# Kernel tuning notes

Measured on AMD Instinct MI355X. Metric: run time of the kernel, lower is better.

## Reference

```python
import jax, jax.numpy as jnp
import numpy as np

N_USERS = 100000
N_ITEMS = 50000
N_NODES = N_USERS + N_ITEMS
EMBED = 64
NNZ = 4000000
BATCH = 4096
N_LAYERS = 3


def setup_inputs() -> dict:
    key = jax.random.key(0)
    k = jax.random.split(key, 8)
    return {
        "batch_user": jax.random.randint(k[0], (BATCH,), 0, N_USERS),
        "batch_pos_item": jax.random.randint(k[1], (BATCH,), 0, N_ITEMS),
        "batch_neg_item": jax.random.randint(k[2], (BATCH,), 0, N_ITEMS),
        "embed_user": jax.random.normal(k[3], (N_USERS, EMBED), dtype=jnp.float32) * 0.1,
        "embed_item": jax.random.normal(k[4], (N_ITEMS, EMBED), dtype=jnp.float32) * 0.1,
        "row_idx": jax.random.randint(k[5], (NNZ,), 0, N_NODES),
        "col_idx": jax.random.randint(k[6], (NNZ,), 0, N_NODES),
        "a_vals": jax.random.uniform(k[7], (NNZ,), dtype=jnp.float32),
    }


def reference(batch_user, batch_pos_item, batch_neg_item,
              embed_user, embed_item, row_idx, col_idx, a_vals):
    # E: [N_NODES, D] stacked user+item embeddings
    E = jnp.concatenate([embed_user, embed_item], axis=0)
    acc = E
    for _ in range(N_LAYERS):
        # SpMM in COO form: out[r] += a[e] * E[c[e]]
        msgs = a_vals[:, None] * E[col_idx]            # [NNZ, D]
        E = jax.ops.segment_sum(msgs, row_idx, num_segments=N_NODES)
        acc = acc + E
    out = acc / (N_LAYERS + 1)
    user_g = out[:N_USERS]
    item_g = out[N_USERS:]
    return (user_g[batch_user], item_g[batch_pos_item], item_g[batch_neg_item])
```

## Files before the change

### kernel.cpp

```cpp
#include <hip/hip_runtime.h>

#define N_USERS 100000
#define N_ITEMS 50000
#define N_NODES 150000
#define EMBED   64
#define NNZV    4000000
#define BATCH   4096
#define BKW     586
#define NBKT    256
#define CAP     18304

__global__ __launch_bounds__(512) void k_parta(
        const int* __restrict__ row, const int* __restrict__ col,
        const float* __restrict__ vals, int* __restrict__ bcnt,
        unsigned long long* __restrict__ staging, int nnz) {
    __shared__ int cnt[NBKT];
    __shared__ int base_s[NBKT];
    int tid = threadIdx.x;
    if (tid < NBKT) cnt[tid] = 0;
    __syncthreads();
    int tile0 = blockIdx.x * 16384;
    for (int k = 0; k < 32; k++) {
        int e = tile0 + k * 512 + tid;
        if (e < nnz) atomicAdd(&cnt[row[e] / BKW], 1);
    }
    __syncthreads();
    if (tid < NBKT) {
        int c_ = cnt[tid];
        base_s[tid] = c_ ? (tid * CAP + atomicAdd(&bcnt[tid], c_)) : 0;
        cnt[tid] = 0;
    }
    __syncthreads();
    for (int k = 0; k < 32; k++) {
        int e = tile0 + k * 512 + tid;
        if (e < nnz) {
            int r = row[e];
            int b = r / BKW;
            int rank = atomicAdd(&cnt[b], 1);
            unsigned int key = ((unsigned int)(r - b * BKW) << 18) | (unsigned int)col[e];
            unsigned long long rec = (unsigned long long)key
                                   | ((unsigned long long)__float_as_uint(vals[e]) << 32);
            staging[base_s[b] + rank] = rec;
        }
    }
}

__global__ __launch_bounds__(512) void k_partb(
        const int* __restrict__ bcnt,
        const unsigned long long* __restrict__ staging,
        int* __restrict__ row_ptr,
        unsigned long long* __restrict__ edges) {
    __shared__ int s[512];
    __shared__ int cnt[BKW];
    __shared__ int cur[BKW];
    __shared__ int base_sh;
    int b = blockIdx.x;
    int t = threadIdx.x;

    int v = (t < NBKT) ? bcnt[t] : 0;
    s[t] = v;
    __syncthreads();
    for (int off = 1; off < 512; off <<= 1) {
        int u = (t >= off) ? s[t - off] : 0;
        __syncthreads();
        s[t] += u;
        __syncthreads();
    }
    if (t == b) base_sh = s[t] - v;
    if (b == 0 && t == 0) row_ptr[N_NODES] = NNZV;
    __syncthreads();
    int base = base_sh;
    int n    = bcnt[b];
    const unsigned long long* sb = staging + (size_t)b * CAP;

    int j0 = 2 * t, j1 = 2 * t + 1;
    if (j0 < BKW) cnt[j0] = 0;
    if (j1 < BKW) cnt[j1] = 0;
    __syncthreads();
    for (int i = t; i < n; i += 512)
        atomicAdd(&cnt[(unsigned int)sb[i] >> 18], 1);
    __syncthreads();
    int c0 = (j0 < BKW) ? cnt[j0] : 0;
    int c1 = (j1 < BKW) ? cnt[j1] : 0;
    int pair = c0 + c1;
    s[t] = pair;
    __syncthreads();
    for (int off = 1; off < 512; off <<= 1) {
        int u = (t >= off) ? s[t - off] : 0;
        __syncthreads();
        s[t] += u;
        __syncthreads();
    }
    int excl = s[t] - pair;
    if (j0 < BKW) cur[j0] = excl;
    if (j1 < BKW) cur[j1] = excl + c0;
    int r0 = b * BKW + j0;
    int r1 = b * BKW + j1;
    if (j0 < BKW && r0 < N_NODES) row_ptr[r0] = base + excl;
    if (j1 < BKW && r1 < N_NODES) row_ptr[r1] = base + excl + c0;
    __syncthreads();
    for (int i = t; i < n; i += 512) {
        unsigned long long rec = sb[i];
        unsigned int key = (unsigned int)rec;
        int rank = atomicAdd(&cur[key >> 18], 1);
        edges[base + rank] = (rec & 0xFFFFFFFF00000000ull) | (key & 0x3FFFFu);
    }
}

__device__ __forceinline__ float4 spmm_row(const int* row_ptr,
                                           const unsigned long long* edges,
                                           const float4* __restrict__ eu4,
                                           const float4* __restrict__ ei4s,
                                           int r, int lane) {
    int g = lane >> 4;
    int d = lane & 15;
    int start = row_ptr[r];
    int end   = row_ptr[r + 1];
    float4 acc = make_float4(0.f, 0.f, 0.f, 0.f);
    for (int e0 = start; e0 < end; e0 += 64) {
        int ei = e0 + lane;
        unsigned long long rec = 0ull;
        if (ei < end) rec = __builtin_nontemporal_load(edges + ei);
        int clo = (int)(rec & 0xffffffffull);
        int vhi = (int)(rec >> 32);
        int nleft = end - e0;
        int kmax = (nleft + 3) >> 2;
        #pragma unroll 4
        for (int k = 0; k < kmax; k++) {
            int src = 4 * k + g;
            int cc = __shfl(clo, src);
            float vv = __int_as_float(__shfl(vhi, src));
            const float4* basep = (cc < N_USERS) ? eu4 : ei4s;
            float4 e = basep[cc * 16 + d];
            acc.x += vv * e.x;
            acc.y += vv * e.y;
            acc.z += vv * e.z;
            acc.w += vv * e.w;
        }
    }
    acc.x += __shfl_xor(acc.x, 16);
    acc.y += __shfl_xor(acc.y, 16);
    acc.z += __shfl_xor(acc.z, 16);
    acc.w += __shfl_xor(acc.w, 16);
    acc.x += __shfl_xor(acc.x, 32);
    acc.y += __shfl_xor(acc.y, 32);
    acc.z += __shfl_xor(acc.z, 32);
    acc.w += __shfl_xor(acc.w, 32);
    return acc;
}

__global__ void k_spmm4(const int* __restrict__ row_ptr,
                        const unsigned long long* __restrict__ edges,
                        const float4* __restrict__ eu4,
                        const float4* __restrict__ ei4s,
                        float4* __restrict__ Eout) {
    int lane = threadIdx.x & 63;
    int wv   = threadIdx.x >> 6;
    int rbase = (blockIdx.x * 4 + wv) * 4;
    if (rbase >= N_NODES) return;
    int g = lane >> 4;
    int d = lane & 15;
    int st[4], en[4], len[4];
    #pragma unroll
    for (int i = 0; i < 4; i++) {
        int r = rbase + i;
        if (r < N_NODES) { st[i] = row_ptr[r]; en[i] = row_ptr[r + 1]; }
        else             { st[i] = 0;          en[i] = 0; }
        len[i] = en[i] - st[i];
    }
    int maxlen = len[0];
    #pragma unroll
    for (int i = 1; i < 4; i++) maxlen = (len[i] > maxlen) ? len[i] : maxlen;

    float4 acc[4];
    #pragma unroll
    for (int i = 0; i < 4; i++) acc[i] = make_float4(0.f, 0.f, 0.f, 0.f);

    for (int off = 0; off < maxlen; off += 64) {
        int clo[4], vhi[4], kmax[4];
        #pragma unroll
        for (int i = 0; i < 4; i++) {
            int ei = st[i] + off + lane;
            unsigned long long rec = 0ull;
            if (ei < en[i]) rec = __builtin_nontemporal_load(edges + ei);
            clo[i] = (int)(rec & 0xffffffffull);
            vhi[i] = (int)(rec >> 32);
            int nleft = len[i] - off;
            if (nleft < 0) nleft = 0; else if (nleft > 64) nleft = 64;
            kmax[i] = (nleft + 3) >> 2;
        }
        int kmx = (maxlen - off + 3) >> 2; if (kmx > 16) kmx = 16;
        #pragma unroll 4
        for (int k = 0; k < kmx; k++) {
            int src = 4 * k + g;
            #pragma unroll
            for (int i = 0; i < 4; i++) {
                if (k < kmax[i]) {
                    int cc = __shfl(clo[i], src);
                    float vv = __int_as_float(__shfl(vhi[i], src));
                    const float4* bp = (cc < N_USERS) ? eu4 : ei4s;
                    float4 e = bp[cc * 16 + d];
                    acc[i].x += vv * e.x;
                    acc[i].y += vv * e.y;
                    acc[i].z += vv * e.z;
                    acc[i].w += vv * e.w;
                }
            }
        }
    }
    #pragma unroll
    for (int i = 0; i < 4; i++) {
        acc[i].x += __shfl_xor(acc[i].x, 16);
        acc[i].y += __shfl_xor(acc[i].y, 16);
        acc[i].z += __shfl_xor(acc[i].z, 16);
        acc[i].w += __shfl_xor(acc[i].w, 16);
        acc[i].x += __shfl_xor(acc[i].x, 32);
        acc[i].y += __shfl_xor(acc[i].y, 32);
        acc[i].z += __shfl_xor(acc[i].z, 32);
        acc[i].w += __shfl_xor(acc[i].w, 32);
    }
    if (lane < 16) {
        #pragma unroll
        for (int i = 0; i < 4; i++)
            if (rbase + i < N_NODES) Eout[(rbase + i) * 16 + lane] = acc[i];
    }
}

__global__ void k_spmm_batch(const int* __restrict__ row_ptr,
                             const unsigned long long* __restrict__ edges,
                             const float4* __restrict__ Ein,
                             const int* __restrict__ bu, const int* __restrict__ bp,
                             const int* __restrict__ bn,
                             float4* __restrict__ out) {
    int lane = threadIdx.x & 63;
    int j = blockIdx.x * 4 + (threadIdx.x >> 6);
    if (j >= 3 * BATCH) return;
    int r;
    if (j < BATCH)          r = bu[j];
    else if (j < 2 * BATCH) r = N_USERS + bp[j - BATCH];
    else                    r = N_USERS + bn[j - 2 * BATCH];
    float4 acc = spmm_row(row_ptr, edges, Ein, Ein, r, lane);
    if (lane < 16) {
        float4 e2 = Ein[r * 16 + lane];
        float4 o  = out[j * 16 + lane];
        o.x += 0.25f * (acc.x + e2.x);
        o.y += 0.25f * (acc.y + e2.y);
        o.z += 0.25f * (acc.z + e2.z);
        o.w += 0.25f * (acc.w + e2.w);
        out[j * 16 + lane] = o;
    }
}

__global__ void k_gather_init(const int* __restrict__ bu, const int* __restrict__ bp,
                              const int* __restrict__ bn,
                              const float4* __restrict__ eu4,
                              const float4* __restrict__ ei4s,
                              float4* __restrict__ out) {
    int idx = blockIdx.x * blockDim.x + threadIdx.x;
    if (idx >= 3 * BATCH * 16) return;
    int j = idx >> 4;
    int d = idx & 15;
    int node;
    if (j < BATCH)          node = bu[j];
    else if (j < 2 * BATCH) node = N_USERS + bp[j - BATCH];
    else                    node = N_USERS + bn[j - 2 * BATCH];
    const float4* basep = (node < N_USERS) ? eu4 : ei4s;
    float4 v = basep[node * 16 + d];
    v.x *= 0.25f; v.y *= 0.25f; v.z *= 0.25f; v.w *= 0.25f;
    out[idx] = v;
}

__global__ void k_gather_acc(const int* __restrict__ bu, const int* __restrict__ bp,
                             const int* __restrict__ bn, const float4* __restrict__ E,
                             float4* __restrict__ out) {
    int idx = blockIdx.x * blockDim.x + threadIdx.x;
    if (idx >= 3 * BATCH * 16) return;
    int j = idx >> 4;
    int d = idx & 15;
    int node;
    if (j < BATCH)          node = bu[j];
    else if (j < 2 * BATCH) node = N_USERS + bp[j - BATCH];
    else                    node = N_USERS + bn[j - 2 * BATCH];
    float4 v = E[node * 16 + d];
    float4 o = out[idx];
    o.x += 0.25f * v.x; o.y += 0.25f * v.y; o.z += 0.25f * v.z; o.w += 0.25f * v.w;
    out[idx] = o;
}

extern "C" void kernel_launch(void* const* d_in, const int* in_sizes, int n_in,
                              void* d_out, int out_size, void* d_ws, size_t ws_size,
                              hipStream_t stream) {
    const int*   bu   = (const int*)d_in[0];
    const int*   bp   = (const int*)d_in[1];
    const int*   bn   = (const int*)d_in[2];
    const float* eu   = (const float*)d_in[3];
    const float* ei   = (const float*)d_in[4];
    const int*   row  = (const int*)d_in[5];
    const int*   col  = (const int*)d_in[6];
    const float* vals = (const float*)d_in[7];
    float* out = (float*)d_out;

    char* p = (char*)d_ws;
    auto alloc = [&](size_t nbytes) {
        void* r = (void*)p;
        p += (nbytes + 255) & ~(size_t)255;
        return r;
    };
    float*              E_a     = (float*)alloc((size_t)N_NODES * EMBED * 4);
    float*              E_b     = (float*)alloc((size_t)N_NODES * EMBED * 4);
    unsigned long long* edges   = (unsigned long long*)alloc((size_t)NNZV * 8);
    int*                row_ptr = (int*)alloc((N_NODES + 1) * 4);
    int*                bcnt    = (int*)alloc(NBKT * 4);
    (void)ws_size; (void)n_in; (void)in_sizes; (void)out_size;

    unsigned long long* staging = (unsigned long long*)E_b;

    const float4* eu4  = (const float4*)eu;
    const float4* ei4s = (const float4*)ei - (size_t)N_USERS * 16;

    const int nnz = NNZV;
    hipMemsetAsync(bcnt, 0, NBKT * sizeof(int), stream);

    k_parta<<<(nnz + 16383) / 16384, 512, 0, stream>>>(row, col, vals, bcnt, staging, nnz);
    k_partb<<<NBKT, 512, 0, stream>>>(bcnt, staging, row_ptr, edges);

    k_gather_init<<<(3 * BATCH * 16 + 255) / 256, 256, 0, stream>>>(
        bu, bp, bn, eu4, ei4s, (float4*)out);

    k_spmm4<<<(N_NODES + 15) / 16, 256, 0, stream>>>(row_ptr, edges, eu4, ei4s,
                                                     (float4*)E_a);
    k_gather_acc<<<(3 * BATCH * 16 + 255) / 256, 256, 0, stream>>>(
        bu, bp, bn, (const float4*)E_a, (float4*)out);

    k_spmm4<<<(N_NODES + 15) / 16, 256, 0, stream>>>(row_ptr, edges,
                                                     (const float4*)E_a,
                                                     (const float4*)E_a,
                                                     (float4*)E_b);

    k_spmm_batch<<<(3 * BATCH + 3) / 4, 256, 0, stream>>>(
        row_ptr, edges, (const float4*)E_b, bu, bp, bn, (float4*)out);
}
```

Before: 507.6 us.

## Double partition buckets and fuse layer-0/1 batch gathers into one kernel

Raises the row-bucket count to 512 with narrower buckets, so k_partb runs 512 blocks with one row per thread instead of 256 blocks with two rows per thread. k_parta now launches one block per bucket, each covering about 7813 edges. The two gather kernels for the initial embeddings and layer-1 output are merged into a single kernel that reads both and writes the output once. This cuts a launch and an output read-modify-write, and the partition steps get more parallelism. In exchange there are more global bucket atomics, and per-bucket capacity now has to hold the edge count of the narrower buckets.

```diff
diff --git a/kernel.cpp b/kernel.cpp
--- a/kernel.cpp
+++ b/kernel.cpp
@@ -6,9 +6,10 @@
 #define EMBED   64
 #define NNZV    4000000
 #define BATCH   4096
-#define BKW     586
-#define NBKT    256
-#define CAP     18304
+#define BKW     293
+#define NBKT    512
+#define CAP     9152
+#define EPB     7813
 
 __global__ __launch_bounds__(512) void k_parta(
         const int* __restrict__ row, const int* __restrict__ col,
@@ -17,23 +18,24 @@
     __shared__ int cnt[NBKT];
     __shared__ int base_s[NBKT];
     int tid = threadIdx.x;
-    if (tid < NBKT) cnt[tid] = 0;
-    __syncthreads();
-    int tile0 = blockIdx.x * 16384;
-    for (int k = 0; k < 32; k++) {
+    cnt[tid] = 0;
+    __syncthreads();
+    int tile0 = blockIdx.x * EPB;
+    int e_end = tile0 + EPB; if (e_end > nnz) e_end = nnz;
+    for (int k = 0; k < 16; k++) {
         int e = tile0 + k * 512 + tid;
-        if (e < nnz) atomicAdd(&cnt[row[e] / BKW], 1);
-    }
-    __syncthreads();
-    if (tid < NBKT) {
+        if (e < e_end) atomicAdd(&cnt[row[e] / BKW], 1);
+    }
+    __syncthreads();
+    {
         int c_ = cnt[tid];
         base_s[tid] = c_ ? (tid * CAP + atomicAdd(&bcnt[tid], c_)) : 0;
         cnt[tid] = 0;
     }
     __syncthreads();
-    for (int k = 0; k < 32; k++) {
+    for (int k = 0; k < 16; k++) {
         int e = tile0 + k * 512 + tid;
-        if (e < nnz) {
+        if (e < e_end) {
             int r = row[e];
             int b = r / BKW;
             int rank = atomicAdd(&cnt[b], 1);
@@ -57,7 +59,7 @@
     int b = blockIdx.x;
     int t = threadIdx.x;
 
-    int v = (t < NBKT) ? bcnt[t] : 0;
+    int v = bcnt[t];
     s[t] = v;
     __syncthreads();
     for (int off = 1; off < 512; off <<= 1) {
@@ -73,17 +75,13 @@
     int n    = bcnt[b];
     const unsigned long long* sb = staging + (size_t)b * CAP;
 
-    int j0 = 2 * t, j1 = 2 * t + 1;
-    if (j0 < BKW) cnt[j0] = 0;
-    if (j1 < BKW) cnt[j1] = 0;
+    if (t < BKW) cnt[t] = 0;
     __syncthreads();
     for (int i = t; i < n; i += 512)
         atomicAdd(&cnt[(unsigned int)sb[i] >> 18], 1);
     __syncthreads();
-    int c0 = (j0 < BKW) ? cnt[j0] : 0;
-    int c1 = (j1 < BKW) ? cnt[j1] : 0;
-    int pair = c0 + c1;
-    s[t] = pair;
+    int c = (t < BKW) ? cnt[t] : 0;
+    s[t] = c;
     __syncthreads();
     for (int off = 1; off < 512; off <<= 1) {
         int u = (t >= off) ? s[t - off] : 0;
@@ -91,13 +89,10 @@
         s[t] += u;
         __syncthreads();
     }
-    int excl = s[t] - pair;
-    if (j0 < BKW) cur[j0] = excl;
-    if (j1 < BKW) cur[j1] = excl + c0;
-    int r0 = b * BKW + j0;
-    int r1 = b * BKW + j1;
-    if (j0 < BKW && r0 < N_NODES) row_ptr[r0] = base + excl;
-    if (j1 < BKW && r1 < N_NODES) row_ptr[r1] = base + excl + c0;
+    int excl = s[t] - c;
+    if (t < BKW) cur[t] = excl;
+    int r = b * BKW + t;
+    if (t < BKW && r < N_NODES) row_ptr[r] = base + excl;
     __syncthreads();
     for (int i = t; i < n; i += 512) {
         unsigned long long rec = sb[i];
@@ -251,11 +246,12 @@
     }
 }
 
-__global__ void k_gather_init(const int* __restrict__ bu, const int* __restrict__ bp,
-                              const int* __restrict__ bn,
-                              const float4* __restrict__ eu4,
-                              const float4* __restrict__ ei4s,
-                              float4* __restrict__ out) {
+__global__ void k_gather2(const int* __restrict__ bu, const int* __restrict__ bp,
+                          const int* __restrict__ bn,
+                          const float4* __restrict__ eu4,
+                          const float4* __restrict__ ei4s,
+                          const float4* __restrict__ E1,
+                          float4* __restrict__ out) {
     int idx = blockIdx.x * blockDim.x + threadIdx.x;
     if (idx >= 3 * BATCH * 16) return;
     int j = idx >> 4;
@@ -265,25 +261,13 @@
     else if (j < 2 * BATCH) node = N_USERS + bp[j - BATCH];
     else                    node = N_USERS + bn[j - 2 * BATCH];
     const float4* basep = (node < N_USERS) ? eu4 : ei4s;
-    float4 v = basep[node * 16 + d];
-    v.x *= 0.25f; v.y *= 0.25f; v.z *= 0.25f; v.w *= 0.25f;
-    out[idx] = v;
-}
-
-__global__ void k_gather_acc(const int* __restrict__ bu, const int* __restrict__ bp,
-                             const int* __restrict__ bn, const float4* __restrict__ E,
-                             float4* __restrict__ out) {
-    int idx = blockIdx.x * blockDim.x + threadIdx.x;
-    if (idx >= 3 * BATCH * 16) return;
-    int j = idx >> 4;
-    int d = idx & 15;
-    int node;
-    if (j < BATCH)          node = bu[j];
-    else if (j < 2 * BATCH) node = N_USERS + bp[j - BATCH];
-    else                    node = N_USERS + bn[j - 2 * BATCH];
-    float4 v = E[node * 16 + d];
-    float4 o = out[idx];
-    o.x += 0.25f * v.x; o.y += 0.25f * v.y; o.z += 0.25f * v.z; o.w += 0.25f * v.w;
+    float4 v0 = basep[node * 16 + d];
+    float4 v1 = E1[node * 16 + d];
+    float4 o;
+    o.x = 0.25f * (v0.x + v1.x);
+    o.y = 0.25f * (v0.y + v1.y);
+    o.z = 0.25f * (v0.z + v1.z);
+    o.w = 0.25f * (v0.w + v1.w);
     out[idx] = o;
 }
 
@@ -321,16 +305,13 @@
     const int nnz = NNZV;
     hipMemsetAsync(bcnt, 0, NBKT * sizeof(int), stream);
 
-    k_parta<<<(nnz + 16383) / 16384, 512, 0, stream>>>(row, col, vals, bcnt, staging, nnz);
+    k_parta<<<NBKT, 512, 0, stream>>>(row, col, vals, bcnt, staging, nnz);
     k_partb<<<NBKT, 512, 0, stream>>>(bcnt, staging, row_ptr, edges);
-
-    k_gather_init<<<(3 * BATCH * 16 + 255) / 256, 256, 0, stream>>>(
-        bu, bp, bn, eu4, ei4s, (float4*)out);
 
     k_spmm4<<<(N_NODES + 15) / 16, 256, 0, stream>>>(row_ptr, edges, eu4, ei4s,
                                                      (float4*)E_a);
-    k_gather_acc<<<(3 * BATCH * 16 + 255) / 256, 256, 0, stream>>>(
-        bu, bp, bn, (const float4*)E_a, (float4*)out);
+    k_gather2<<<(3 * BATCH * 16 + 255) / 256, 256, 0, stream>>>(
+        bu, bp, bn, eu4, ei4s, (const float4*)E_a, (float4*)out);
 
     k_spmm4<<<(N_NODES + 15) / 16, 256, 0, stream>>>(row_ptr, edges,
                                                      (const float4*)E_a,
```

After: 523.1 us. +3.1%, slower.
